# Kernel tuning notes

Measured on AMD Instinct MI355X. Metric: run time of the kernel, lower is better.

The kernel has to match this reference:

```python
import jax, jax.numpy as jnp
import numpy as np

B, T, V, S_FIXED, DIM, CV = 4, 256, 1024, 64, 1024, 256


def setup_inputs() -> dict:
    key = jax.random.key(0)
    ks = jax.random.split(key, 8)
    x = jax.random.normal(ks[0], (B, T, DIM), jnp.float32)
    vision = jax.random.normal(ks[1], (B, V, CV), jnp.float32)
    # attention mask (B, V, T): each text token t attends to exactly S_FIXED vision tokens
    scores = jax.random.uniform(ks[2], (B, T, V))
    _, sel = jax.lax.top_k(scores, S_FIXED)  # (B, T, S)
    mask_tv = jnp.zeros((B, T, V), bool)
    mask_tv = mask_tv.at[jnp.arange(B)[:, None, None], jnp.arange(T)[None, :, None], sel].set(True)
    attention_mask = jnp.transpose(mask_tv, (0, 2, 1))  # (B, V, T)
    # xavier-uniform-like params (scale irrelevant for correctness baseline)
    Wu = jax.random.normal(ks[3], (CV, DIM), jnp.float32) * (1.0 / np.sqrt(CV))
    bu = jax.random.normal(ks[4], (DIM,), jnp.float32) * 0.02
    Wk = jax.random.normal(ks[5], (DIM, DIM), jnp.float32) * (1.0 / np.sqrt(DIM))
    Wv = jax.random.normal(ks[6], (DIM, DIM), jnp.float32) * (1.0 / np.sqrt(DIM))
    return {"x": x, "vision": vision, "attention_mask": attention_mask,
            "Wu": Wu, "bu": bu, "Wk": Wk, "Wv": Wv, "S": S_FIXED}


def reference(x, vision, attention_mask, Wu, bu, Wk, Wv, S):
    Bv, Vn, Cv = vision.shape
    Bx, Tn, C = x.shape  # C == dim
    # --- _construct_sparse_inputs ---
    mask_tv = jnp.transpose(attention_mask, (0, 2, 1))  # (B, T, V)
    idx_full = jnp.where(mask_tv, jnp.arange(Vn, dtype=jnp.int32), jnp.int32(Vn))
    # topk(largest=False) == smallest S indices, ascending; pad value = Vn
    index = -jax.lax.top_k(-idx_full, S)[0]  # (B, T, S)
    vision_pad = jnp.concatenate([vision, jnp.zeros((Bv, 1, Cv), vision.dtype)], axis=1)  # (B, V+1, Cv)
    vg = jnp.take_along_axis(vision_pad, index.reshape(Bv, Tn * S, 1), axis=1)
    vg = vg.reshape(Bv, Tn, S, Cv)  # (B, T, S, 256)
    # NOTE: faithful to source — VALID positions receive the -100 bias
    mask_qk = (index != Vn)[..., None].astype(jnp.float32) * (-100.0)  # (B, T, S, 1)
    # --- attention ---
    vu = vg @ Wu + bu           # (B, T, S, dim)
    k = vu @ Wk                 # (B, T, S, dim)
    v = vu @ Wv                 # (B, T, S, dim)
    q = x[:, :, None, :]        # (B, T, 1, dim)
    qk = jnp.einsum('bksc,bktc->bkst', k, q) / jnp.sqrt(jnp.float32(C)) + mask_qk  # (B, T, S, 1)
    sm = jax.nn.softmax(qk.reshape(Bx, -1), axis=-1).reshape(qk.shape)  # softmax over flattened T*S*1
    attn = jnp.einsum('bkst,bksc->bktc', sm, v)  # (B, T, 1, dim)
    return (attn + q).squeeze(2)  # (B, T, dim)
```

## Files before the change

### kernel.cpp

```cpp
#include <hip/hip_runtime.h>
#include <stdint.h>

#define B 4
#define T 256
#define V 1024
#define S 64
#define DIM 1024
#define CV 256

typedef __attribute__((ext_vector_type(8))) short bf16x8;
typedef __attribute__((ext_vector_type(4))) short s16x4;
typedef __attribute__((ext_vector_type(4))) float f32x4;

enum : int {
    WKT_O   = 0,
    WVT_O   = WKT_O + 262144,
    WUB_O   = WVT_O + 262144,
    WKPB_O  = WUB_O + 131072,
    WVPT_O  = WKPB_O + 131072,
    XB_O    = WVPT_O + 131072,
    ZB_O    = XB_O + 262144,
    VB_O    = ZB_O + 131072,
    WB_O    = VB_O + 524288,
    RS_O    = WB_O + 131072,
    PIDX_O  = RS_O + B*T,
    BK_O    = PIDX_O + B*T*S,
    BV_O    = BK_O + DIM,
    BP_O    = BV_O + DIM,
    WS_TOTAL= BP_O + 2*16*1024
};

__device__ __forceinline__ short f2bf(float f) {
    union { float f; unsigned u; } x; x.f = f;
    unsigned r = (x.u + 0x7FFF + ((x.u >> 16) & 1)) >> 16;
    return (short)r;
}
__device__ __forceinline__ float bf2f(short s) {
    union { unsigned u; float f; } x;
    x.u = ((unsigned)(unsigned short)s) << 16;
    return x.f;
}
__device__ __forceinline__ s16x4 cvt4(float4 f) {
    s16x4 o;
    o.x = f2bf(f.x); o.y = f2bf(f.y); o.z = f2bf(f.z); o.w = f2bf(f.w);
    return o;
}

__global__ void stage1(const float* __restrict__ vision, const float* __restrict__ Wu,
                       const float* __restrict__ x, const float* __restrict__ Wk,
                       const float* __restrict__ Wv, const float* __restrict__ bu,
                       const void* __restrict__ maskp,
                       float* __restrict__ ws, int* __restrict__ wsi) {
    __shared__ short tlds[64 * 65];
    __shared__ float tred[4 * 64];
    __shared__ int mc_cnt[16][17];
    __shared__ int sa_flag, sb_flag;
    int blk = blockIdx.x;
    int tid = threadIdx.x;

    if (blk < 2304) {
        const float* src; short* dst; int idx;
        if (blk < 1024)      { src = vision; dst = (short*)(ws + VB_O);  idx = blk; }
        else if (blk < 1280) { src = Wu;     dst = (short*)(ws + WUB_O); idx = blk - 1024; }
        else                 { src = x;      dst = (short*)(ws + XB_O);  idx = blk - 1280; }
        int i = (idx * 256 + tid);
        ((s16x4*)dst)[i] = cvt4(((const float4*)src)[i]);
        return;
    }
    if (blk < 2816) {
        int tile = blk - 2304;
        int which = tile >> 8, t2 = tile & 255;
        int e0 = (t2 >> 4) * 64, d0 = (t2 & 15) * 64;
        const float* src = which ? Wv : Wk;
        short* dst = (short*)(ws + (which ? WVT_O : WKT_O));
        int j = tid & 63, i0 = tid >> 6;
        float pb = 0.f;
#pragma unroll
        for (int p = 0; p < 16; p++) {
            int i = p * 4 + i0;
            float v = src[(size_t)(e0 + i) * DIM + d0 + j];
            tlds[j * 65 + i] = f2bf(v);
            pb += bu[e0 + i] * v;
        }
        tred[i0 * 64 + j] = pb;
        __syncthreads();
#pragma unroll
        for (int p = 0; p < 16; p++) {
            int dd = p * 4 + i0;
            dst[(size_t)(d0 + dd) * DIM + e0 + j] = tlds[dd * 65 + j];
        }
        if (i0 == 0) {
            float s = tred[j] + tred[64 + j] + tred[128 + j] + tred[192 + j];
            ws[BP_O + (which * 16 + (e0 >> 6)) * 1024 + d0 + j] = s;
        }
        return;
    }
    {
        int a = 0, bfl = 0;
        const uchar4* m4 = (const uchar4*)maskp;
#pragma unroll
        for (int jj = 0; jj < 4; jj++) {
            uchar4 u = m4[tid * 4 + jj];
            if (u.y | u.z | u.w) a = 1;
            if (u.x == 0x3f || u.y == 0x3f || u.z == 0x3f || u.w == 0x3f) bfl = 1;
        }
        if (tid == 0) { sa_flag = 0; sb_flag = 0; }
        __syncthreads();
        if (a) sa_flag = 1;
        if (bfl) sb_flag = 1;
        __syncthreads();
    }
    bool byteMode = sa_flag && !sb_flag;
    int mb = blk - 2816;
    int b = mb >> 4, tg = mb & 15;
    int tl = tid & 15, c = tid >> 4;
    int t = tg * 16 + tl;
    int v0 = c * 64;
    unsigned long long bits = 0ull;
    if (byteMode) {
        const uint8_t* m = (const uint8_t*)maskp + (size_t)(b * V + v0) * T + t;
#pragma unroll 8
        for (int j = 0; j < 64; j++)
            if (m[(size_t)j * T] != 0) bits |= 1ull << j;
    } else {
        const int* m = (const int*)maskp + (size_t)(b * V + v0) * T + t;
#pragma unroll 8
        for (int j = 0; j < 64; j++)
            if (m[(size_t)j * T] != 0) bits |= 1ull << j;
    }
    mc_cnt[tl][c] = __popcll(bits);
    __syncthreads();
    int off = 0, total = 0;
#pragma unroll
    for (int cc = 0; cc < 16; cc++) {
        int cn = mc_cnt[tl][cc];
        if (cc < c) off += cn;
        total += cn;
    }
    int base = PIDX_O + (b * T + t) * S;
    while (bits) {
        int j = __ffsll(bits) - 1;
        bits &= bits - 1;
        if (off < S) wsi[base + off] = v0 + j;
        off++;
    }
    if (c == 15)
        for (int j = (total < S ? total : S); j < S; j++) wsi[base + j] = 0;
}

template<int K, int LDA, int LDB>
__device__ __forceinline__ void wave_mma(const short* __restrict__ A0,
                                         const short* __restrict__ B0,
                                         f32x4 acc[2][2]) {
    int lane = threadIdx.x & 63;
    int rw = lane & 15, q = lane >> 4;
    const short* ap0 = A0 + rw * LDA + q * 8;
    const short* ap1 = ap0 + 16 * LDA;
    const short* bp0 = B0 + rw * LDB + q * 8;
    const short* bp1 = bp0 + 16 * LDB;
#pragma unroll 4
    for (int kc = 0; kc < K; kc += 32) {
        bf16x8 a0 = *(const bf16x8*)(ap0 + kc);
        bf16x8 a1 = *(const bf16x8*)(ap1 + kc);
        bf16x8 b0 = *(const bf16x8*)(bp0 + kc);
        bf16x8 b1 = *(const bf16x8*)(bp1 + kc);
        acc[0][0] = __builtin_amdgcn_mfma_f32_16x16x32_bf16(a0, b0, acc[0][0], 0, 0, 0);
        acc[0][1] = __builtin_amdgcn_mfma_f32_16x16x32_bf16(a0, b1, acc[0][1], 0, 0, 0);
        acc[1][0] = __builtin_amdgcn_mfma_f32_16x16x32_bf16(a1, b0, acc[1][0], 0, 0, 0);
        acc[1][1] = __builtin_amdgcn_mfma_f32_16x16x32_bf16(a1, b1, acc[1][1], 0, 0, 0);
    }
}

__global__ void g_prep_mfma(float* __restrict__ ws) {
    if (blockIdx.x >= 128) {
        int which = blockIdx.x - 128;
#pragma unroll
        for (int cch = 0; cch < 4; cch++) {
            int d = cch * 256 + threadIdx.x;
            float s = 0.f;
#pragma unroll
            for (int g = 0; g < 16; g++)
                s += ws[BP_O + (which * 16 + g) * 1024 + d];
            ws[(which ? BV_O : BK_O) + d] = s;
        }
        return;
    }
    int w = blockIdx.x * 4 + (threadIdx.x >> 6);
    int which = w >> 8, rem = w & 255;
    int m0 = (rem >> 5) * 32, n0 = (rem & 31) * 32;
    const short* A = (const short*)(ws + WUB_O) + (size_t)m0 * DIM;
    const short* Bt = (const short*)(ws + (which ? WVT_O : WKT_O)) + (size_t)n0 * DIM;
    f32x4 acc[2][2] = {};
    wave_mma<DIM, DIM, DIM>(A, Bt, acc);
    int lane = threadIdx.x & 63, col = lane & 15, q = lane >> 4;
    if (which == 0) {
        short* o = (short*)(ws + WKPB_O);
#pragma unroll
        for (int i = 0; i < 2; i++)
#pragma unroll
            for (int j = 0; j < 2; j++)
#pragma unroll
                for (int r = 0; r < 4; r++)
                    o[(size_t)(m0 + i * 16 + q * 4 + r) * DIM + n0 + j * 16 + col] =
                        f2bf(acc[i][j][r]);
    } else {
        short* o = (short*)(ws + WVPT_O);
#pragma unroll
        for (int i = 0; i < 2; i++)
#pragma unroll
            for (int j = 0; j < 2; j++) {
                s16x4 v;
                v.x = f2bf(acc[i][j][0]); v.y = f2bf(acc[i][j][1]);
                v.z = f2bf(acc[i][j][2]); v.w = f2bf(acc[i][j][3]);
                *(s16x4*)&o[(size_t)(n0 + j * 16 + col) * CV + m0 + i * 16 + q * 4] = v;
            }
    }
}

__global__ void g_z_mfma(float* __restrict__ ws) {
    int w = blockIdx.x * 4 + (threadIdx.x >> 6);
    int m0 = (w >> 3) * 32, n0 = (w & 7) * 32;
    const short* A = (const short*)(ws + XB_O) + (size_t)m0 * DIM;
    const short* Bt = (const short*)(ws + WKPB_O) + (size_t)n0 * DIM;
    f32x4 acc[2][2] = {};
    wave_mma<DIM, DIM, DIM>(A, Bt, acc);
    int lane = threadIdx.x & 63, col = lane & 15, q = lane >> 4;
    short* zb = (short*)(ws + ZB_O);
#pragma unroll
    for (int i = 0; i < 2; i++)
#pragma unroll
        for (int j = 0; j < 2; j++)
#pragma unroll
            for (int r = 0; r < 4; r++)
                zb[(size_t)(m0 + i * 16 + q * 4 + r) * CV + n0 + j * 16 + col] =
                    f2bf(acc[i][j][r]);
}

__global__ void g_attn(const float* __restrict__ x, float* __restrict__ ws,
                       int* __restrict__ wsi) {
    __shared__ int s_idx[4][64];
    __shared__ float s_ps[4][64];
    int tid = threadIdx.x;
    int lane = tid & 63, wv = tid >> 6;
    int bt = blockIdx.x * 4 + wv, b = bt >> 8;
    s_idx[wv][lane] = wsi[PIDX_O + bt * S + lane];
    float c0p = 0.f;
    const float4* xr = (const float4*)(x + (size_t)bt * DIM);
    const float4* bkr = (const float4*)(ws + BK_O);
#pragma unroll
    for (int j = 0; j < 4; j++) {
        float4 a = xr[lane + 64 * j], k4 = bkr[lane + 64 * j];
        c0p += a.x * k4.x + a.y * k4.y + a.z * k4.z + a.w * k4.w;
    }
    for (int o = 32; o > 0; o >>= 1) c0p += __shfl_xor(c0p, o);
    float c0 = c0p;
    int rw = lane & 15, q = lane >> 4;
    const short* vb = (const short*)(ws + VB_O) + (size_t)b * V * CV;
    const short* zp = (const short*)(ws + ZB_O) + (size_t)bt * CV + q * 8;
    f32x4 acc[4] = {};
#pragma unroll
    for (int mt = 0; mt < 4; mt++) {
        const short* ap = vb + (size_t)s_idx[wv][mt * 16 + rw] * CV + q * 8;
        f32x4 a4 = {0.f, 0.f, 0.f, 0.f};
#pragma unroll
        for (int kc = 0; kc < CV; kc += 32) {
            bf16x8 av = *(const bf16x8*)(ap + kc);
            bf16x8 bv = *(const bf16x8*)(zp + kc);
            a4 = __builtin_amdgcn_mfma_f32_16x16x32_bf16(av, bv, a4, 0, 0, 0);
        }
        acc[mt] = a4;
    }
    if (rw == 0) {
#pragma unroll
        for (int mt = 0; mt < 4; mt++)
#pragma unroll
            for (int r = 0; r < 4; r++)
                s_ps[wv][mt * 16 + q * 4 + r] = acc[mt][r];
    }
    float p = expf((s_ps[wv][lane] + c0) * 0.03125f);
    float rs = p;
    for (int o = 32; o > 0; o >>= 1) rs += __shfl_xor(rs, o);
    s_ps[wv][lane] = p;
    if (lane == 0) ws[RS_O + bt] = rs;
    float4 wa = {0.f, 0.f, 0.f, 0.f};
#pragma unroll 8
    for (int s = 0; s < S; s++) {
        float pv = s_ps[wv][s];
        s16x4 r4 = *(const s16x4*)(vb + (size_t)s_idx[wv][s] * CV + lane * 4);
        wa.x += pv * bf2f(r4.x); wa.y += pv * bf2f(r4.y);
        wa.z += pv * bf2f(r4.z); wa.w += pv * bf2f(r4.w);
    }
    s16x4 o;
    o.x = f2bf(wa.x); o.y = f2bf(wa.y); o.z = f2bf(wa.z); o.w = f2bf(wa.w);
    ((s16x4*)((short*)(ws + WB_O) + (size_t)bt * CV))[lane] = o;
}

__global__ void g_out_mfma(const float* __restrict__ x, float* __restrict__ ws,
                           float* __restrict__ out) {
    int w = blockIdx.x * 4 + (threadIdx.x >> 6);
    int m0 = (w >> 5) * 32, n0 = (w & 31) * 32;
    int lane = threadIdx.x & 63;
    int b = m0 >> 8;
    float4 r4 = *(const float4*)(ws + RS_O + b * 256 + lane * 4);
    float dn = r4.x + r4.y + r4.z + r4.w;
    for (int o = 32; o > 0; o >>= 1) dn += __shfl_xor(dn, o);
    float inv = 1.0f / dn;
    const short* A = (const short*)(ws + WB_O) + (size_t)m0 * CV;
    const short* Bt = (const short*)(ws + WVPT_O) + (size_t)n0 * CV;
    f32x4 acc[2][2] = {};
    wave_mma<CV, CV, CV>(A, Bt, acc);
    int col = lane & 15, q = lane >> 4;
#pragma unroll
    for (int i = 0; i < 2; i++)
#pragma unroll
        for (int r = 0; r < 4; r++) {
            int row = m0 + i * 16 + q * 4 + r;
            float rs = ws[RS_O + row];
#pragma unroll
            for (int j = 0; j < 2; j++) {
                int cc = n0 + j * 16 + col;
                out[(size_t)row * DIM + cc] =
                    x[(size_t)row * DIM + cc] +
                    (acc[i][j][r] + rs * ws[BV_O + cc]) * inv;
            }
        }
}

extern "C" void kernel_launch(void* const* d_in, const int* in_sizes, int n_in,
                              void* d_out, int out_size, void* d_ws, size_t ws_size,
                              hipStream_t stream) {
    (void)in_sizes; (void)n_in; (void)out_size; (void)ws_size;
    const float* x      = (const float*)d_in[0];
    const float* vision = (const float*)d_in[1];
    const void*  mask   = d_in[2];
    const float* Wu     = (const float*)d_in[3];
    const float* bu     = (const float*)d_in[4];
    const float* Wk     = (const float*)d_in[5];
    const float* Wv     = (const float*)d_in[6];
    float* out = (float*)d_out;
    float* ws  = (float*)d_ws;
    int*   wsi = (int*)d_ws;

    stage1<<<2880, 256, 0, stream>>>(vision, Wu, x, Wk, Wv, bu, mask, ws, wsi);
    g_prep_mfma<<<130, 256, 0, stream>>>(ws);
    g_z_mfma<<<64, 256, 0, stream>>>(ws);
    g_attn<<<256, 256, 0, stream>>>(x, ws, wsi);
    g_out_mfma<<<256, 256, 0, stream>>>(x, ws, out);
}
```

Before: 140.7 us.

## Project vision tokens to full dim instead of folding Wu into Wk/Wv

Replaces the precomputed Wu·Wk / Wu·Wv factorization with a direct projection vu = vision@Wu+bu for all vision tokens and y = x@Wkᵀ. Attention then runs in the 1024-wide space, and the output GEMM multiplies by transposed Wv. This folds the conversion, projection and mask-compaction work into one launch, so five kernels become three and the bias-correction terms go away. In exchange, the gathered rows in the attention kernel are four times wider and the output GEMM has a larger K, which adds cache and memory traffic.

```diff
diff --git a/kernel.cpp b/kernel.cpp
--- a/kernel.cpp
+++ b/kernel.cpp
@@ -13,21 +13,13 @@
 typedef __attribute__((ext_vector_type(4))) float f32x4;
 
 enum : int {
-    WKT_O   = 0,
-    WVT_O   = WKT_O + 262144,
-    WUB_O   = WVT_O + 262144,
-    WKPB_O  = WUB_O + 131072,
-    WVPT_O  = WKPB_O + 131072,
-    XB_O    = WVPT_O + 131072,
-    ZB_O    = XB_O + 262144,
-    VB_O    = ZB_O + 131072,
-    WB_O    = VB_O + 524288,
-    RS_O    = WB_O + 131072,
-    PIDX_O  = RS_O + B*T,
-    BK_O    = PIDX_O + B*T*S,
-    BV_O    = BK_O + DIM,
-    BP_O    = BV_O + DIM,
-    WS_TOTAL= BP_O + 2*16*1024
+    VUB_O  = 0,
+    YB_O   = VUB_O + 2097152,
+    WVT_O  = YB_O + 524288,
+    UB_O   = WVT_O + 524288,
+    RS_O   = UB_O + 524288,
+    PIDX_O = RS_O + B*T,
+    WS_TOTAL = PIDX_O + B*T*S
 };
 
 __device__ __forceinline__ short f2bf(float f) {
@@ -40,112 +32,13 @@
     x.u = ((unsigned)(unsigned short)s) << 16;
     return x.f;
 }
-__device__ __forceinline__ s16x4 cvt4(float4 f) {
-    s16x4 o;
-    o.x = f2bf(f.x); o.y = f2bf(f.y); o.z = f2bf(f.z); o.w = f2bf(f.w);
-    return o;
-}
-
-__global__ void stage1(const float* __restrict__ vision, const float* __restrict__ Wu,
-                       const float* __restrict__ x, const float* __restrict__ Wk,
-                       const float* __restrict__ Wv, const float* __restrict__ bu,
-                       const void* __restrict__ maskp,
-                       float* __restrict__ ws, int* __restrict__ wsi) {
-    __shared__ short tlds[64 * 65];
-    __shared__ float tred[4 * 64];
-    __shared__ int mc_cnt[16][17];
-    __shared__ int sa_flag, sb_flag;
-    int blk = blockIdx.x;
-    int tid = threadIdx.x;
-
-    if (blk < 2304) {
-        const float* src; short* dst; int idx;
-        if (blk < 1024)      { src = vision; dst = (short*)(ws + VB_O);  idx = blk; }
-        else if (blk < 1280) { src = Wu;     dst = (short*)(ws + WUB_O); idx = blk - 1024; }
-        else                 { src = x;      dst = (short*)(ws + XB_O);  idx = blk - 1280; }
-        int i = (idx * 256 + tid);
-        ((s16x4*)dst)[i] = cvt4(((const float4*)src)[i]);
-        return;
-    }
-    if (blk < 2816) {
-        int tile = blk - 2304;
-        int which = tile >> 8, t2 = tile & 255;
-        int e0 = (t2 >> 4) * 64, d0 = (t2 & 15) * 64;
-        const float* src = which ? Wv : Wk;
-        short* dst = (short*)(ws + (which ? WVT_O : WKT_O));
-        int j = tid & 63, i0 = tid >> 6;
-        float pb = 0.f;
-#pragma unroll
-        for (int p = 0; p < 16; p++) {
-            int i = p * 4 + i0;
-            float v = src[(size_t)(e0 + i) * DIM + d0 + j];
-            tlds[j * 65 + i] = f2bf(v);
-            pb += bu[e0 + i] * v;
-        }
-        tred[i0 * 64 + j] = pb;
-        __syncthreads();
-#pragma unroll
-        for (int p = 0; p < 16; p++) {
-            int dd = p * 4 + i0;
-            dst[(size_t)(d0 + dd) * DIM + e0 + j] = tlds[dd * 65 + j];
-        }
-        if (i0 == 0) {
-            float s = tred[j] + tred[64 + j] + tred[128 + j] + tred[192 + j];
-            ws[BP_O + (which * 16 + (e0 >> 6)) * 1024 + d0 + j] = s;
-        }
-        return;
-    }
-    {
-        int a = 0, bfl = 0;
-        const uchar4* m4 = (const uchar4*)maskp;
-#pragma unroll
-        for (int jj = 0; jj < 4; jj++) {
-            uchar4 u = m4[tid * 4 + jj];
-            if (u.y | u.z | u.w) a = 1;
-            if (u.x == 0x3f || u.y == 0x3f || u.z == 0x3f || u.w == 0x3f) bfl = 1;
-        }
-        if (tid == 0) { sa_flag = 0; sb_flag = 0; }
-        __syncthreads();
-        if (a) sa_flag = 1;
-        if (bfl) sb_flag = 1;
-        __syncthreads();
-    }
-    bool byteMode = sa_flag && !sb_flag;
-    int mb = blk - 2816;
-    int b = mb >> 4, tg = mb & 15;
-    int tl = tid & 15, c = tid >> 4;
-    int t = tg * 16 + tl;
-    int v0 = c * 64;
-    unsigned long long bits = 0ull;
-    if (byteMode) {
-        const uint8_t* m = (const uint8_t*)maskp + (size_t)(b * V + v0) * T + t;
-#pragma unroll 8
-        for (int j = 0; j < 64; j++)
-            if (m[(size_t)j * T] != 0) bits |= 1ull << j;
-    } else {
-        const int* m = (const int*)maskp + (size_t)(b * V + v0) * T + t;
-#pragma unroll 8
-        for (int j = 0; j < 64; j++)
-            if (m[(size_t)j * T] != 0) bits |= 1ull << j;
-    }
-    mc_cnt[tl][c] = __popcll(bits);
-    __syncthreads();
-    int off = 0, total = 0;
-#pragma unroll
-    for (int cc = 0; cc < 16; cc++) {
-        int cn = mc_cnt[tl][cc];
-        if (cc < c) off += cn;
-        total += cn;
-    }
-    int base = PIDX_O + (b * T + t) * S;
-    while (bits) {
-        int j = __ffsll(bits) - 1;
-        bits &= bits - 1;
-        if (off < S) wsi[base + off] = v0 + j;
-        off++;
-    }
-    if (c == 15)
-        for (int j = (total < S ? total : S); j < S; j++) wsi[base + j] = 0;
+__device__ __forceinline__ bf16x8 ld_cvt8(const float* __restrict__ p) {
+    float4 f0 = *(const float4*)p;
+    float4 f1 = *(const float4*)(p + 4);
+    bf16x8 r;
+    r[0] = f2bf(f0.x); r[1] = f2bf(f0.y); r[2] = f2bf(f0.z); r[3] = f2bf(f0.w);
+    r[4] = f2bf(f1.x); r[5] = f2bf(f1.y); r[6] = f2bf(f1.z); r[7] = f2bf(f1.w);
+    return r;
 }
 
 template<int K, int LDA, int LDB>
@@ -171,101 +64,186 @@
     }
 }
 
-__global__ void g_prep_mfma(float* __restrict__ ws) {
-    if (blockIdx.x >= 128) {
-        int which = blockIdx.x - 128;
-#pragma unroll
-        for (int cch = 0; cch < 4; cch++) {
-            int d = cch * 256 + threadIdx.x;
-            float s = 0.f;
-#pragma unroll
-            for (int g = 0; g < 16; g++)
-                s += ws[BP_O + (which * 16 + g) * 1024 + d];
-            ws[(which ? BV_O : BK_O) + d] = s;
-        }
+__global__ void k1(const float* __restrict__ vision, const float* __restrict__ Wu,
+                   const float* __restrict__ bu, const float* __restrict__ x,
+                   const float* __restrict__ Wk, const float* __restrict__ Wv,
+                   const void* __restrict__ maskp,
+                   float* __restrict__ ws, int* __restrict__ wsi) {
+    __shared__ short smem[64 * 264];
+    int blk = blockIdx.x, tid = threadIdx.x;
+    int lane = tid & 63, wvi = tid >> 6;
+    int rw = lane & 15, q = lane >> 4;
+
+    if (blk < 1024) {
+        int m0 = (blk >> 4) * 64, n0 = (blk & 15) * 64;
+#pragma unroll
+        for (int p = 0; p < 16; p++) {
+            int f4 = p * 256 + tid;
+            int cv = f4 >> 4, c4 = (f4 & 15) * 4;
+            float4 w = ((const float4*)(Wu + (size_t)cv * DIM + n0))[f4 & 15];
+            smem[(c4 + 0) * 264 + cv] = f2bf(w.x);
+            smem[(c4 + 1) * 264 + cv] = f2bf(w.y);
+            smem[(c4 + 2) * 264 + cv] = f2bf(w.z);
+            smem[(c4 + 3) * 264 + cv] = f2bf(w.w);
+        }
+        __syncthreads();
+        int wm = (wvi >> 1) * 32, wn = (wvi & 1) * 32;
+        const float* a0p = vision + (size_t)(m0 + wm + rw) * CV + q * 8;
+        const float* a1p = a0p + 16 * CV;
+        const short* b0p = smem + (wn + rw) * 264 + q * 8;
+        const short* b1p = b0p + 16 * 264;
+        f32x4 acc[2][2] = {};
+#pragma unroll
+        for (int kc = 0; kc < CV; kc += 32) {
+            bf16x8 a0 = ld_cvt8(a0p + kc);
+            bf16x8 a1 = ld_cvt8(a1p + kc);
+            bf16x8 b0 = *(const bf16x8*)(b0p + kc);
+            bf16x8 b1 = *(const bf16x8*)(b1p + kc);
+            acc[0][0] = __builtin_amdgcn_mfma_f32_16x16x32_bf16(a0, b0, acc[0][0], 0, 0, 0);
+            acc[0][1] = __builtin_amdgcn_mfma_f32_16x16x32_bf16(a0, b1, acc[0][1], 0, 0, 0);
+            acc[1][0] = __builtin_amdgcn_mfma_f32_16x16x32_bf16(a1, b0, acc[1][0], 0, 0, 0);
+            acc[1][1] = __builtin_amdgcn_mfma_f32_16x16x32_bf16(a1, b1, acc[1][1], 0, 0, 0);
+        }
+        int col = lane & 15;
+        short* vub = (short*)(ws + VUB_O);
+        float bu0 = bu[n0 + wn + col], bu1 = bu[n0 + wn + 16 + col];
+#pragma unroll
+        for (int i = 0; i < 2; i++)
+#pragma unroll
+            for (int j = 0; j < 2; j++) {
+                float badd = j ? bu1 : bu0;
+#pragma unroll
+                for (int r = 0; r < 4; r++) {
+                    int vr = m0 + wm + i * 16 + q * 4 + r;
+                    int e  = n0 + wn + j * 16 + col;
+                    vub[(size_t)vr * DIM + e] = f2bf(acc[i][j][r] + badd);
+                }
+            }
         return;
     }
-    int w = blockIdx.x * 4 + (threadIdx.x >> 6);
-    int which = w >> 8, rem = w & 255;
-    int m0 = (rem >> 5) * 32, n0 = (rem & 31) * 32;
-    const short* A = (const short*)(ws + WUB_O) + (size_t)m0 * DIM;
-    const short* Bt = (const short*)(ws + (which ? WVT_O : WKT_O)) + (size_t)n0 * DIM;
-    f32x4 acc[2][2] = {};
-    wave_mma<DIM, DIM, DIM>(A, Bt, acc);
-    int lane = threadIdx.x & 63, col = lane & 15, q = lane >> 4;
-    if (which == 0) {
-        short* o = (short*)(ws + WKPB_O);
+    if (blk < 1280) {
+        int b2 = blk - 1024;
+        int m0 = (b2 >> 4) * 64, n0 = (b2 & 15) * 64;
+        int wm = (wvi >> 1) * 32, wn = (wvi & 1) * 32;
+        const float* a0p = x + (size_t)(m0 + wm + rw) * DIM + q * 8;
+        const float* a1p = a0p + 16 * DIM;
+        const float* b0p = Wk + (size_t)(n0 + wn + rw) * DIM + q * 8;
+        const float* b1p = b0p + 16 * DIM;
+        f32x4 acc[2][2] = {};
+#pragma unroll 4
+        for (int kc = 0; kc < DIM; kc += 32) {
+            bf16x8 a0 = ld_cvt8(a0p + kc);
+            bf16x8 a1 = ld_cvt8(a1p + kc);
+            bf16x8 b0 = ld_cvt8(b0p + kc);
+            bf16x8 b1 = ld_cvt8(b1p + kc);
+            acc[0][0] = __builtin_amdgcn_mfma_f32_16x16x32_bf16(a0, b0, acc[0][0], 0, 0, 0);
+            acc[0][1] = __builtin_amdgcn_mfma_f32_16x16x32_bf16(a0, b1, acc[0][1], 0, 0, 0);
+            acc[1][0] = __builtin_amdgcn_mfma_f32_16x16x32_bf16(a1, b0, acc[1][0], 0, 0, 0);
+            acc[1][1] = __builtin_amdgcn_mfma_f32_16x16x32_bf16(a1, b1, acc[1][1], 0, 0, 0);
+        }
+        int col = lane & 15;
+        short* yb = (short*)(ws + YB_O);
 #pragma unroll
         for (int i = 0; i < 2; i++)
 #pragma unroll
             for (int j = 0; j < 2; j++)
 #pragma unroll
                 for (int r = 0; r < 4; r++)
-                    o[(size_t)(m0 + i * 16 + q * 4 + r) * DIM + n0 + j * 16 + col] =
-                        f2bf(acc[i][j][r]);
+                    yb[(size_t)(m0 + wm + i * 16 + q * 4 + r) * DIM +
+                       n0 + wn + j * 16 + col] = f2bf(acc[i][j][r]);
+        return;
+    }
+    if (blk < 1536) {
+        int t2 = blk - 1280;
+        int e0 = (t2 >> 4) * 64, d0 = (t2 & 15) * 64;
+        short* tl = smem;
+        short* dst = (short*)(ws + WVT_O);
+        int j = tid & 63, i0 = tid >> 6;
+#pragma unroll
+        for (int p = 0; p < 16; p++) {
+            int i = p * 4 + i0;
+            tl[j * 65 + i] = f2bf(Wv[(size_t)(e0 + i) * DIM + d0 + j]);
+        }
+        __syncthreads();
+#pragma unroll
+        for (int p = 0; p < 16; p++) {
+            int dd = p * 4 + i0;
+            dst[(size_t)(d0 + dd) * DIM + e0 + j] = tl[dd * 65 + j];
+        }
+        return;
+    }
+    int* si = (int*)smem;
+    {
+        int a = 0, bfl = 0;
+        const uchar4* m4 = (const uchar4*)maskp;
+#pragma unroll
+        for (int jj = 0; jj < 4; jj++) {
+            uchar4 u = m4[tid * 4 + jj];
+            if (u.y | u.z | u.w) a = 1;
+            if (u.x == 0x3f || u.y == 0x3f || u.z == 0x3f || u.w == 0x3f) bfl = 1;
+        }
+        if (tid == 0) { si[272] = 0; si[273] = 0; }
+        __syncthreads();
+        if (a) si[272] = 1;
+        if (bfl) si[273] = 1;
+        __syncthreads();
+    }
+    bool byteMode = si[272] && !si[273];
+    int mb = blk - 1536;
+    int b = mb >> 4, tg = mb & 15;
+    int tl2 = tid & 15, c = tid >> 4;
+    int t = tg * 16 + tl2;
+    int v0 = c * 64;
+    unsigned long long bits = 0ull;
+    if (byteMode) {
+        const uint8_t* m = (const uint8_t*)maskp + (size_t)(b * V + v0) * T + t;
+#pragma unroll 8
+        for (int j = 0; j < 64; j++)
+            if (m[(size_t)j * T] != 0) bits |= 1ull << j;
     } else {
-        short* o = (short*)(ws + WVPT_O);
-#pragma unroll
-        for (int i = 0; i < 2; i++)
-#pragma unroll
-            for (int j = 0; j < 2; j++) {
-                s16x4 v;
-                v.x = f2bf(acc[i][j][0]); v.y = f2bf(acc[i][j][1]);
-                v.z = f2bf(acc[i][j][2]); v.w = f2bf(acc[i][j][3]);
-                *(s16x4*)&o[(size_t)(n0 + j * 16 + col) * CV + m0 + i * 16 + q * 4] = v;
-            }
-    }
-}
-
-__global__ void g_z_mfma(float* __restrict__ ws) {
-    int w = blockIdx.x * 4 + (threadIdx.x >> 6);
-    int m0 = (w >> 3) * 32, n0 = (w & 7) * 32;
-    const short* A = (const short*)(ws + XB_O) + (size_t)m0 * DIM;
-    const short* Bt = (const short*)(ws + WKPB_O) + (size_t)n0 * DIM;
-    f32x4 acc[2][2] = {};
-    wave_mma<DIM, DIM, DIM>(A, Bt, acc);
-    int lane = threadIdx.x & 63, col = lane & 15, q = lane >> 4;
-    short* zb = (short*)(ws + ZB_O);
-#pragma unroll
-    for (int i = 0; i < 2; i++)
-#pragma unroll
-        for (int j = 0; j < 2; j++)
-#pragma unroll
-            for (int r = 0; r < 4; r++)
-                zb[(size_t)(m0 + i * 16 + q * 4 + r) * CV + n0 + j * 16 + col] =
-                    f2bf(acc[i][j][r]);
-}
-
-__global__ void g_attn(const float* __restrict__ x, float* __restrict__ ws,
-                       int* __restrict__ wsi) {
+        const int* m = (const int*)maskp + (size_t)(b * V + v0) * T + t;
+#pragma unroll 8
+        for (int j = 0; j < 64; j++)
+            if (m[(size_t)j * T] != 0) bits |= 1ull << j;
+    }
+    si[tl2 * 17 + c] = __popcll(bits);
+    __syncthreads();
+    int off = 0, total = 0;
+#pragma unroll
+    for (int cc = 0; cc < 16; cc++) {
+        int cn = si[tl2 * 17 + cc];
+        if (cc < c) off += cn;
+        total += cn;
+    }
+    int base = PIDX_O + (b * T + t) * S;
+    while (bits) {
+        int j = __ffsll(bits) - 1;
+        bits &= bits - 1;
+        if (off < S) wsi[base + off] = v0 + j;
+        off++;
+    }
+    if (c == 15)
+        for (int j = (total < S ? total : S); j < S; j++) wsi[base + j] = 0;
+}
+
+__global__ void g_attn(float* __restrict__ ws, int* __restrict__ wsi) {
     __shared__ int s_idx[4][64];
     __shared__ float s_ps[4][64];
-    int tid = threadIdx.x;
-    int lane = tid & 63, wv = tid >> 6;
-    int bt = blockIdx.x * 4 + wv, b = bt >> 8;
-    s_idx[wv][lane] = wsi[PIDX_O + bt * S + lane];
-    float c0p = 0.f;
-    const float4* xr = (const float4*)(x + (size_t)bt * DIM);
-    const float4* bkr = (const float4*)(ws + BK_O);
-#pragma unroll
-    for (int j = 0; j < 4; j++) {
-        float4 a = xr[lane + 64 * j], k4 = bkr[lane + 64 * j];
-        c0p += a.x * k4.x + a.y * k4.y + a.z * k4.z + a.w * k4.w;
-    }
-    for (int o = 32; o > 0; o >>= 1) c0p += __shfl_xor(c0p, o);
-    float c0 = c0p;
+    int tid = threadIdx.x, lane = tid & 63, wvi = tid >> 6;
+    int bt = blockIdx.x * 4 + wvi, b = bt >> 8;
+    s_idx[wvi][lane] = wsi[PIDX_O + bt * S + lane];
     int rw = lane & 15, q = lane >> 4;
-    const short* vb = (const short*)(ws + VB_O) + (size_t)b * V * CV;
-    const short* zp = (const short*)(ws + ZB_O) + (size_t)bt * CV + q * 8;
+    const short* vub = (const short*)(ws + VUB_O);
+    const short* yp = (const short*)(ws + YB_O) + (size_t)bt * DIM + q * 8;
     f32x4 acc[4] = {};
 #pragma unroll
     for (int mt = 0; mt < 4; mt++) {
-        const short* ap = vb + (size_t)s_idx[wv][mt * 16 + rw] * CV + q * 8;
+        const short* ap = vub + (size_t)(b * V + s_idx[wvi][mt * 16 + rw]) * DIM + q * 8;
         f32x4 a4 = {0.f, 0.f, 0.f, 0.f};
-#pragma unroll
-        for (int kc = 0; kc < CV; kc += 32) {
+#pragma unroll 8
+        for (int kc = 0; kc < DIM; kc += 32) {
             bf16x8 av = *(const bf16x8*)(ap + kc);
-            bf16x8 bv = *(const bf16x8*)(zp + kc);
+            bf16x8 bv = *(const bf16x8*)(yp + kc);
             a4 = __builtin_amdgcn_mfma_f32_16x16x32_bf16(av, bv, a4, 0, 0, 0);
         }
         acc[mt] = a4;
@@ -275,24 +253,33 @@
         for (int mt = 0; mt < 4; mt++)
 #pragma unroll
             for (int r = 0; r < 4; r++)
-                s_ps[wv][mt * 16 + q * 4 + r] = acc[mt][r];
-    }
-    float p = expf((s_ps[wv][lane] + c0) * 0.03125f);
+                s_ps[wvi][mt * 16 + q * 4 + r] = acc[mt][r];
+    }
+    float p = expf(s_ps[wvi][lane] * 0.03125f);
     float rs = p;
     for (int o = 32; o > 0; o >>= 1) rs += __shfl_xor(rs, o);
-    s_ps[wv][lane] = p;
+    s_ps[wvi][lane] = p;
     if (lane == 0) ws[RS_O + bt] = rs;
-    float4 wa = {0.f, 0.f, 0.f, 0.f};
-#pragma unroll 8
+    float4 u[4] = {};
+#pragma unroll 4
     for (int s = 0; s < S; s++) {
-        float pv = s_ps[wv][s];
-        s16x4 r4 = *(const s16x4*)(vb + (size_t)s_idx[wv][s] * CV + lane * 4);
-        wa.x += pv * bf2f(r4.x); wa.y += pv * bf2f(r4.y);
-        wa.z += pv * bf2f(r4.z); wa.w += pv * bf2f(r4.w);
-    }
-    s16x4 o;
-    o.x = f2bf(wa.x); o.y = f2bf(wa.y); o.z = f2bf(wa.z); o.w = f2bf(wa.w);
-    ((s16x4*)((short*)(ws + WB_O) + (size_t)bt * CV))[lane] = o;
+        float pv = s_ps[wvi][s];
+        const short* vr = vub + (size_t)(b * V + s_idx[wvi][s]) * DIM;
+#pragma unroll
+        for (int jj = 0; jj < 4; jj++) {
+            s16x4 r4 = *(const s16x4*)(vr + jj * 256 + lane * 4);
+            u[jj].x += pv * bf2f(r4.x); u[jj].y += pv * bf2f(r4.y);
+            u[jj].z += pv * bf2f(r4.z); u[jj].w += pv * bf2f(r4.w);
+        }
+    }
+    short* ub = (short*)(ws + UB_O) + (size_t)bt * DIM;
+#pragma unroll
+    for (int jj = 0; jj < 4; jj++) {
+        s16x4 o;
+        o.x = f2bf(u[jj].x); o.y = f2bf(u[jj].y);
+        o.z = f2bf(u[jj].z); o.w = f2bf(u[jj].w);
+        *(s16x4*)(ub + jj * 256 + lane * 4) = o;
+    }
 }
 
 __global__ void g_out_mfma(const float* __restrict__ x, float* __restrict__ ws,
@@ -305,23 +292,21 @@
     float dn = r4.x + r4.y + r4.z + r4.w;
     for (int o = 32; o > 0; o >>= 1) dn += __shfl_xor(dn, o);
     float inv = 1.0f / dn;
-    const short* A = (const short*)(ws + WB_O) + (size_t)m0 * CV;
-    const short* Bt = (const short*)(ws + WVPT_O) + (size_t)n0 * CV;
+    const short* A = (const short*)(ws + UB_O) + (size_t)m0 * DIM;
+    const short* Bt = (const short*)(ws + WVT_O) + (size_t)n0 * DIM;
     f32x4 acc[2][2] = {};
-    wave_mma<CV, CV, CV>(A, Bt, acc);
+    wave_mma<DIM, DIM, DIM>(A, Bt, acc);
     int col = lane & 15, q = lane >> 4;
 #pragma unroll
     for (int i = 0; i < 2; i++)
 #pragma unroll
         for (int r = 0; r < 4; r++) {
             int row = m0 + i * 16 + q * 4 + r;
-            float rs = ws[RS_O + row];
 #pragma unroll
             for (int j = 0; j < 2; j++) {
                 int cc = n0 + j * 16 + col;
                 out[(size_t)row * DIM + cc] =
-                    x[(size_t)row * DIM + cc] +
-                    (acc[i][j][r] + rs * ws[BV_O + cc]) * inv;
+                    x[(size_t)row * DIM + cc] + acc[i][j][r] * inv;
             }
         }
 }
@@ -341,9 +326,7 @@
     float* ws  = (float*)d_ws;
     int*   wsi = (int*)d_ws;
 
-    stage1<<<2880, 256, 0, stream>>>(vision, Wu, x, Wk, Wv, bu, mask, ws, wsi);
-    g_prep_mfma<<<130, 256, 0, stream>>>(ws);
-    g_z_mfma<<<64, 256, 0, stream>>>(ws);
-    g_attn<<<256, 256, 0, stream>>>(x, ws, wsi);
+    k1<<<1600, 256, 0, stream>>>(vision, Wu, bu, x, Wk, Wv, mask, ws, wsi);
+    g_attn<<<256, 256, 0, stream>>>(ws, wsi);
     g_out_mfma<<<256, 256, 0, stream>>>(x, ws, out);
 }
```

Measured after the change: 188.2 us. +33.8%, slower.

## Fuse the z projection GEMM into the attention kernel via shared memory

Applied to the files above, without the earlier changes.

Removes the separate g_z_mfma launch and computes each block's four rows of z = x·Wkp inside g_attn with MFMA, storing them in LDS rather than round-tripping through global memory. This saves one kernel launch and the global write and read of z. In exchange, the MFMA tile is padded to 16 columns while only 4 text rows are real, so most of that MMA work is wasted, and each block rereads the whole Wkp matrix. Workspace offsets are also rearranged and ZB is dropped.

```diff
diff --git a/kernel.cpp b/kernel.cpp
--- a/kernel.cpp
+++ b/kernel.cpp
@@ -13,21 +13,20 @@
 typedef __attribute__((ext_vector_type(4))) float f32x4;
 
 enum : int {
-    WKT_O   = 0,
-    WVT_O   = WKT_O + 262144,
-    WUB_O   = WVT_O + 262144,
-    WKPB_O  = WUB_O + 131072,
-    WVPT_O  = WKPB_O + 131072,
-    XB_O    = WVPT_O + 131072,
-    ZB_O    = XB_O + 262144,
-    VB_O    = ZB_O + 131072,
-    WB_O    = VB_O + 524288,
-    RS_O    = WB_O + 131072,
-    PIDX_O  = RS_O + B*T,
-    BK_O    = PIDX_O + B*T*S,
-    BV_O    = BK_O + DIM,
-    BP_O    = BV_O + DIM,
-    WS_TOTAL= BP_O + 2*16*1024
+    WKT_O  = 0,
+    WVT_O  = WKT_O + 524288,
+    WUB_O  = WVT_O + 524288,
+    WKPB_O = WUB_O + 131072,
+    WVPT_O = WKPB_O + 131072,
+    XB_O   = WVPT_O + 131072,
+    VB_O   = XB_O + 524288,
+    WB_O   = VB_O + 524288,
+    RS_O   = WB_O + 131072,
+    PIDX_O = RS_O + B*T,
+    BK_O   = PIDX_O + B*T*S,
+    BV_O   = BK_O + DIM,
+    BP_O   = BV_O + DIM,
+    WS_TOTAL = BP_O + 2*16*1024
 };
 
 __device__ __forceinline__ short f2bf(float f) {
@@ -63,7 +62,7 @@
         if (blk < 1024)      { src = vision; dst = (short*)(ws + VB_O);  idx = blk; }
         else if (blk < 1280) { src = Wu;     dst = (short*)(ws + WUB_O); idx = blk - 1024; }
         else                 { src = x;      dst = (short*)(ws + XB_O);  idx = blk - 1280; }
-        int i = (idx * 256 + tid);
+        int i = idx * 256 + tid;
         ((s16x4*)dst)[i] = cvt4(((const float4*)src)[i]);
         return;
     }
@@ -217,33 +216,43 @@
     }
 }
 
-__global__ void g_z_mfma(float* __restrict__ ws) {
-    int w = blockIdx.x * 4 + (threadIdx.x >> 6);
-    int m0 = (w >> 3) * 32, n0 = (w & 7) * 32;
-    const short* A = (const short*)(ws + XB_O) + (size_t)m0 * DIM;
-    const short* Bt = (const short*)(ws + WKPB_O) + (size_t)n0 * DIM;
-    f32x4 acc[2][2] = {};
-    wave_mma<DIM, DIM, DIM>(A, Bt, acc);
-    int lane = threadIdx.x & 63, col = lane & 15, q = lane >> 4;
-    short* zb = (short*)(ws + ZB_O);
-#pragma unroll
-    for (int i = 0; i < 2; i++)
-#pragma unroll
-        for (int j = 0; j < 2; j++)
-#pragma unroll
-            for (int r = 0; r < 4; r++)
-                zb[(size_t)(m0 + i * 16 + q * 4 + r) * CV + n0 + j * 16 + col] =
-                    f2bf(acc[i][j][r]);
-}
-
 __global__ void g_attn(const float* __restrict__ x, float* __restrict__ ws,
                        int* __restrict__ wsi) {
+    __shared__ short zs[4][256];
     __shared__ int s_idx[4][64];
     __shared__ float s_ps[4][64];
-    int tid = threadIdx.x;
-    int lane = tid & 63, wv = tid >> 6;
-    int bt = blockIdx.x * 4 + wv, b = bt >> 8;
+    int tid = threadIdx.x, lane = tid & 63, wv = tid >> 6;
+    int bt0 = blockIdx.x * 4;
+    int bt = bt0 + wv, b = bt >> 8;
+    int rw = lane & 15, q = lane >> 4;
     s_idx[wv][lane] = wsi[PIDX_O + bt * S + lane];
+
+    {
+        const short* xb = (const short*)(ws + XB_O);
+        const short* wkp = (const short*)(ws + WKPB_O);
+        const short* bp = xb + (size_t)(bt0 + rw) * DIM + q * 8;
+#pragma unroll
+        for (int tt = 0; tt < 4; tt++) {
+            int m0 = wv * 64 + tt * 16;
+            const short* ap = wkp + (size_t)(m0 + rw) * DIM + q * 8;
+            f32x4 a4 = {0.f, 0.f, 0.f, 0.f};
+#pragma unroll 8
+            for (int kc = 0; kc < DIM; kc += 32) {
+                bf16x8 av = *(const bf16x8*)(ap + kc);
+                bf16x8 bv = *(const bf16x8*)(bp + kc);
+                a4 = __builtin_amdgcn_mfma_f32_16x16x32_bf16(av, bv, a4, 0, 0, 0);
+            }
+            int col = lane & 15;
+            if (col < 4) {
+                s16x4 v;
+                v.x = f2bf(a4[0]); v.y = f2bf(a4[1]);
+                v.z = f2bf(a4[2]); v.w = f2bf(a4[3]);
+                *(s16x4*)&zs[col][m0 + q * 4] = v;
+            }
+        }
+    }
+    __syncthreads();
+
     float c0p = 0.f;
     const float4* xr = (const float4*)(x + (size_t)bt * DIM);
     const float4* bkr = (const float4*)(ws + BK_O);
@@ -254,9 +263,8 @@
     }
     for (int o = 32; o > 0; o >>= 1) c0p += __shfl_xor(c0p, o);
     float c0 = c0p;
-    int rw = lane & 15, q = lane >> 4;
     const short* vb = (const short*)(ws + VB_O) + (size_t)b * V * CV;
-    const short* zp = (const short*)(ws + ZB_O) + (size_t)bt * CV + q * 8;
+    const short* zp = &zs[wv][q * 8];
     f32x4 acc[4] = {};
 #pragma unroll
     for (int mt = 0; mt < 4; mt++) {
@@ -343,7 +351,6 @@
 
     stage1<<<2880, 256, 0, stream>>>(vision, Wu, x, Wk, Wv, bu, mask, ws, wsi);
     g_prep_mfma<<<130, 256, 0, stream>>>(ws);
-    g_z_mfma<<<64, 256, 0, stream>>>(ws);
     g_attn<<<256, 256, 0, stream>>>(x, ws, wsi);
     g_out_mfma<<<256, 256, 0, stream>>>(x, ws, out);
 }
```

Measured after the change: 149.1 us. +6.0%, slower.
